# Kernel optimization log

Hardware: AMD Instinct MI355X
Metric: run time of the kernel (lower is better)

## Reference

```python
import jax, jax.numpy as jnp
import numpy as np

EMBED_DIM = 1024
NUM_HEADS = 16
HEAD_DIM = EMBED_DIM // NUM_HEADS


def setup_inputs() -> dict:
    key = jax.random.key(0)
    ks = jax.random.split(key, 11)
    B, S, E = 4, 2048, EMBED_DIM
    s = 1.0 / np.sqrt(E)
    return {
        "q": jax.random.normal(ks[0], (B, S, E), jnp.float32),
        "k": jax.random.normal(ks[1], (B, S, E), jnp.float32),
        "v": jax.random.normal(ks[2], (B, S, E), jnp.float32),
        "Wq": jax.random.uniform(ks[3], (E, E), jnp.float32, -s, s),
        "bq": jax.random.uniform(ks[4], (E,), jnp.float32, -s, s),
        "Wk": jax.random.uniform(ks[5], (E, E), jnp.float32, -s, s),
        "bk": jax.random.uniform(ks[6], (E,), jnp.float32, -s, s),
        "Wv": jax.random.uniform(ks[7], (E, E), jnp.float32, -s, s),
        "bv": jax.random.uniform(ks[8], (E,), jnp.float32, -s, s),
        "Wo": jax.random.uniform(ks[9], (E, E), jnp.float32, -s, s),
        "bo": jax.random.uniform(ks[10], (E,), jnp.float32, -s, s),
    }


def _split_heads(x):
    B, S, E = x.shape
    return x.reshape(B, S, NUM_HEADS, HEAD_DIM).transpose(0, 2, 1, 3)  # [B,H,S,D]


def reference(q, k, v, Wq, bq, Wk, bk, Wv, bv, Wo, bo):
    # torch Linear: x @ W.T + b
    Q = _split_heads(q @ Wq.T + bq)
    K = _split_heads(k @ Wk.T + bk)
    V = _split_heads(v @ Wv.T + bv)
    scale = 1.0 / jnp.sqrt(jnp.float32(HEAD_DIM))
    scores = jnp.einsum("bhqd,bhkd->bhqk", Q, K) * scale  # [B,H,S,S]
    weights = jax.nn.softmax(scores, axis=-1)
    ctx = jnp.einsum("bhqk,bhkd->bhqd", weights, V)
    B, H, S, D = ctx.shape
    merged = ctx.transpose(0, 2, 1, 3).reshape(B, S, H * D)
    out = merged @ Wo.T + bo
    return out, weights
```

## Files before the change

kernel.cpp:

```cpp
#include <hip/hip_runtime.h>
#include <hip/hip_bf16.h>

typedef __bf16 bf16x8 __attribute__((ext_vector_type(8)));
typedef float f32x4 __attribute__((ext_vector_type(4)));

constexpr size_t XQ_OFF = 0;
constexpr size_t XK_OFF = 8388608;
constexpr size_t XV_OFF = 16777216;
constexpr size_t WQ_OFF = 25165824;
constexpr size_t WK_OFF = 26214400;
constexpr size_t WV_OFF = 27262976;
constexpr size_t WO_OFF = 28311552;
constexpr size_t Q_OFF  = 29360128;
constexpr size_t KK_OFF = 37748736;
constexpr size_t VT_OFF = 46137344;
constexpr size_t CTX_OFF= 54525952;

__device__ __forceinline__ void gload16(const void* g, void* s) {
    __builtin_amdgcn_global_load_lds((__attribute__((address_space(1))) void*)g,
                                     (__attribute__((address_space(3))) void*)s, 16, 0, 0);
}

__global__ __launch_bounds__(256) void convert_k(
    const float* __restrict__ q, const float* __restrict__ k, const float* __restrict__ v,
    const float* __restrict__ Wq, const float* __restrict__ Wk, const float* __restrict__ Wv,
    const float* __restrict__ Wo, __bf16* __restrict__ ws) {
    int id = blockIdx.x * 256 + threadIdx.x;
    const int NX = 1048576;
    const int NW = 131072;
    const float* src; size_t dst; int local;
    if (id < 3 * NX) {
        int z = id / NX; local = id - z * NX;
        src = (z == 0) ? q : ((z == 1) ? k : v);
        dst = XQ_OFF + (size_t)z * 8388608;
    } else {
        int i2 = id - 3 * NX;
        int z = i2 / NW; local = i2 - z * NW;
        src = (z == 0) ? Wq : ((z == 1) ? Wk : ((z == 2) ? Wv : Wo));
        dst = WQ_OFF + (size_t)z * 1048576;
    }
    const float4* s4 = (const float4*)(src + (size_t)local * 8);
    float4 a = s4[0], b = s4[1];
    bf16x8 o;
    o[0]=(__bf16)a.x; o[1]=(__bf16)a.y; o[2]=(__bf16)a.z; o[3]=(__bf16)a.w;
    o[4]=(__bf16)b.x; o[5]=(__bf16)b.y; o[6]=(__bf16)b.z; o[7]=(__bf16)b.w;
    *(bf16x8*)(ws + dst + (size_t)local * 8) = o;
}

template<int MODE>
__global__ __launch_bounds__(256) void gemm_k(
    __bf16* __restrict__ ws,
    const float* __restrict__ bq, const float* __restrict__ bk,
    const float* __restrict__ bv, const float* __restrict__ bo,
    float* __restrict__ out) {
    const int K = 1024;
    int z = blockIdx.z;
    const __bf16* A; const __bf16* Bm; const float* bias;
    if (MODE == 0) {
        A    = ws + XQ_OFF + (size_t)z * 8388608;
        Bm   = ws + WQ_OFF + (size_t)z * 1048576;
        bias = (z == 0) ? bq : ((z == 1) ? bk : bv);
    } else {
        A    = ws + CTX_OFF;
        Bm   = ws + WO_OFF;
        bias = bo;
    }
    int row0 = blockIdx.x * 128, col0 = blockIdx.y * 128;
    __shared__ __align__(16) __bf16 As[128 * 32];
    __shared__ __align__(16) __bf16 Bs[128 * 32];
    int t = threadIdx.x, lane = t & 63, w = t >> 6;
    int wr = w >> 1, wc = w & 1;
    f32x4 acc[4][4];
#pragma unroll
    for (int i = 0; i < 4; ++i)
#pragma unroll
        for (int j = 0; j < 4; ++j) acc[i][j] = (f32x4){0.f, 0.f, 0.f, 0.f};

    for (int kt = 0; kt < K; kt += 32) {
#pragma unroll
        for (int i = 0; i < 2; ++i) {
            int e = ((i * 4 + w) * 64 + lane) * 8;
            int r = e >> 5, c = e & 31;
            gload16(A  + (size_t)(row0 + r) * K + kt + c, As + e);
            gload16(Bm + (size_t)(col0 + r) * K + kt + c, Bs + e);
        }
        __syncthreads();
        bf16x8 af[4], bfr[4];
#pragma unroll
        for (int f = 0; f < 4; ++f) {
            af[f]  = *(const bf16x8*)&As[(wr * 64 + f * 16 + (lane & 15)) * 32 + (lane >> 4) * 8];
            bfr[f] = *(const bf16x8*)&Bs[(wc * 64 + f * 16 + (lane & 15)) * 32 + (lane >> 4) * 8];
        }
#pragma unroll
        for (int fr = 0; fr < 4; ++fr)
#pragma unroll
            for (int fc = 0; fc < 4; ++fc)
                acc[fr][fc] = __builtin_amdgcn_mfma_f32_16x16x32_bf16(af[fr], bfr[fc], acc[fr][fc], 0, 0, 0);
        __syncthreads();
    }

    if (MODE == 0) {
        __bf16* dqk = ws + Q_OFF + (size_t)z * 8388608;
        __bf16* dvt = ws + VT_OFF;
#pragma unroll
        for (int fr = 0; fr < 4; ++fr)
#pragma unroll
            for (int fc = 0; fc < 4; ++fc)
#pragma unroll
                for (int r = 0; r < 4; ++r) {
                    int m = row0 + wr * 64 + fr * 16 + ((lane >> 4) << 2) + r;
                    int n = col0 + wc * 64 + fc * 16 + (lane & 15);
                    float val = acc[fr][fc][r] + bias[n];
                    int bb = m >> 11, s = m & 2047, h = n >> 6, d = n & 63;
                    size_t bh = (size_t)bb * 16 + h;
                    if (z < 2) dqk[bh * 131072 + (size_t)s * 64 + d] = (__bf16)val;
                    else       dvt[bh * 131072 + (size_t)d * 2048 + s] = (__bf16)val;
                }
    } else {
#pragma unroll
        for (int fr = 0; fr < 4; ++fr)
#pragma unroll
            for (int fc = 0; fc < 4; ++fc)
#pragma unroll
                for (int r = 0; r < 4; ++r) {
                    int m = row0 + wr * 64 + fr * 16 + ((lane >> 4) << 2) + r;
                    int n = col0 + wc * 64 + fc * 16 + (lane & 15);
                    out[(size_t)m * 1024 + n] = acc[fr][fc][r] + bias[n];
                }
    }
}

__global__ __launch_bounds__(256) void attn_k(const __bf16* __restrict__ ws,
                                              __bf16* __restrict__ wsw,
                                              float* __restrict__ wout) {
    const __bf16* Qp  = ws + Q_OFF;
    const __bf16* Kp  = ws + KK_OFF;
    const __bf16* Vtp = ws + VT_OFF;
    __bf16* ctx = wsw + CTX_OFF;

    int bh = blockIdx.y;
    int q0 = blockIdx.x * 64;
    int t = threadIdx.x, lane = t & 63, w = t >> 6;
    __shared__ __align__(16) __bf16 Qs[64 * 64];
    __shared__ __align__(16) __bf16 Ks[64 * 64];
    __shared__ __align__(16) __bf16 Vts[64 * 64];
    __shared__ __align__(16) __bf16 Ps[64 * 64];
    const float SCALE = 0.125f;

#pragma unroll
    for (int i = 0; i < 2; ++i) {
        int ch = t + 256 * i;
        int r = ch >> 3, c8 = ch & 7;
        bf16x8 val = *(const bf16x8*)&Qp[(size_t)bh * 131072 + (size_t)(q0 + r) * 64 + c8 * 8];
        *(bf16x8*)((char*)Qs + (r * 128 + ((c8 * 16) ^ ((r & 7) << 4)))) = val;
    }
    __syncthreads();
    int qrow = w * 16 + (lane & 15);
    bf16x8 aq0 = *(const bf16x8*)((char*)Qs + (qrow * 128 + (((lane >> 4) * 16)      ^ ((qrow & 7) << 4))));
    bf16x8 aq1 = *(const bf16x8*)((char*)Qs + (qrow * 128 + ((64 + (lane >> 4) * 16) ^ ((qrow & 7) << 4))));

    float rs[4] = {0.f, 0.f, 0.f, 0.f};
    for (int kt = 0; kt < 2048; kt += 64) {
        __syncthreads();
#pragma unroll
        for (int i = 0; i < 2; ++i) {
            int ch = t + 256 * i; int r = ch >> 3, c8 = ch & 7;
            bf16x8 val = *(const bf16x8*)&Kp[(size_t)bh * 131072 + (size_t)(kt + r) * 64 + c8 * 8];
            *(bf16x8*)((char*)Ks + (r * 128 + ((c8 * 16) ^ ((r & 7) << 4)))) = val;
        }
        __syncthreads();
#pragma unroll
        for (int kc = 0; kc < 4; ++kc) {
            int krow = kc * 16 + (lane & 15);
            bf16x8 b0 = *(const bf16x8*)((char*)Ks + (krow * 128 + (((lane >> 4) * 16)      ^ ((krow & 7) << 4))));
            bf16x8 b1 = *(const bf16x8*)((char*)Ks + (krow * 128 + ((64 + (lane >> 4) * 16) ^ ((krow & 7) << 4))));
            f32x4 s = (f32x4){0.f, 0.f, 0.f, 0.f};
            s = __builtin_amdgcn_mfma_f32_16x16x32_bf16(aq0, b0, s, 0, 0, 0);
            s = __builtin_amdgcn_mfma_f32_16x16x32_bf16(aq1, b1, s, 0, 0, 0);
#pragma unroll
            for (int r = 0; r < 4; ++r) rs[r] += __expf(s[r] * SCALE);
        }
    }
#pragma unroll
    for (int m = 1; m < 16; m <<= 1)
#pragma unroll
        for (int r = 0; r < 4; ++r) rs[r] += __shfl_xor(rs[r], m, 64);
    float rinv[4];
#pragma unroll
    for (int r = 0; r < 4; ++r) rinv[r] = 1.f / rs[r];

    f32x4 cacc[4];
#pragma unroll
    for (int i = 0; i < 4; ++i) cacc[i] = (f32x4){0.f, 0.f, 0.f, 0.f};

    for (int kt = 0; kt < 2048; kt += 64) {
        __syncthreads();
#pragma unroll
        for (int i = 0; i < 2; ++i) {
            int ch = t + 256 * i; int r = ch >> 3, c8 = ch & 7;
            bf16x8 kv = *(const bf16x8*)&Kp[(size_t)bh * 131072 + (size_t)(kt + r) * 64 + c8 * 8];
            *(bf16x8*)((char*)Ks + (r * 128 + ((c8 * 16) ^ ((r & 7) << 4)))) = kv;
            bf16x8 vv = *(const bf16x8*)&Vtp[(size_t)bh * 131072 + (size_t)r * 2048 + kt + c8 * 8];
            *(bf16x8*)((char*)Vts + (r * 128 + ((c8 * 16) ^ ((r & 7) << 4)))) = vv;
        }
        __syncthreads();
#pragma unroll
        for (int kc = 0; kc < 4; ++kc) {
            int krow = kc * 16 + (lane & 15);
            bf16x8 b0 = *(const bf16x8*)((char*)Ks + (krow * 128 + (((lane >> 4) * 16)      ^ ((krow & 7) << 4))));
            bf16x8 b1 = *(const bf16x8*)((char*)Ks + (krow * 128 + ((64 + (lane >> 4) * 16) ^ ((krow & 7) << 4))));
            f32x4 s = (f32x4){0.f, 0.f, 0.f, 0.f};
            s = __builtin_amdgcn_mfma_f32_16x16x32_bf16(aq0, b0, s, 0, 0, 0);
            s = __builtin_amdgcn_mfma_f32_16x16x32_bf16(aq1, b1, s, 0, 0, 0);
            float e[4];
#pragma unroll
            for (int r = 0; r < 4; ++r) e[r] = __expf(s[r] * SCALE) * rinv[r];
            size_t wbase = ((size_t)bh * 2048 + q0 + w * 16 + ((lane >> 4) << 2)) * 2048
                           + kt + kc * 16 + (lane & 15);
#pragma unroll
            for (int r = 0; r < 4; ++r) wout[wbase + (size_t)r * 2048] = e[r];
#pragma unroll
            for (int r = 0; r < 4; ++r) {
                int prow = w * 16 + ((lane >> 4) << 2) + r;
                int pcol = kc * 16 + (lane & 15);
                *(__bf16*)((char*)Ps + (prow * 128 + ((pcol * 2) ^ ((prow & 7) << 4)))) = (__bf16)e[r];
            }
        }
        __syncthreads();
#pragma unroll
        for (int ks = 0; ks < 2; ++ks) {
            int arow = w * 16 + (lane & 15);
            bf16x8 ap = *(const bf16x8*)((char*)Ps + (arow * 128 + ((ks * 64 + (lane >> 4) * 16) ^ ((arow & 7) << 4))));
#pragma unroll
            for (int dc = 0; dc < 4; ++dc) {
                int vrow = dc * 16 + (lane & 15);
                bf16x8 bv = *(const bf16x8*)((char*)Vts + (vrow * 128 + ((ks * 64 + (lane >> 4) * 16) ^ ((vrow & 7) << 4))));
                cacc[dc] = __builtin_amdgcn_mfma_f32_16x16x32_bf16(ap, bv, cacc[dc], 0, 0, 0);
            }
        }
    }

    int bb = bh >> 4, h = bh & 15;
#pragma unroll
    for (int dc = 0; dc < 4; ++dc)
#pragma unroll
        for (int r = 0; r < 4; ++r) {
            int qg = q0 + w * 16 + ((lane >> 4) << 2) + r;
            int d = dc * 16 + (lane & 15);
            ctx[((size_t)bb * 2048 + qg) * 1024 + h * 64 + d] = (__bf16)cacc[dc][r];
        }
}

extern "C" void kernel_launch(void* const* d_in, const int* in_sizes, int n_in,
                              void* d_out, int out_size, void* d_ws, size_t ws_size,
                              hipStream_t stream) {
    const float* q  = (const float*)d_in[0];
    const float* k  = (const float*)d_in[1];
    const float* v  = (const float*)d_in[2];
    const float* Wq = (const float*)d_in[3];
    const float* bq = (const float*)d_in[4];
    const float* Wk = (const float*)d_in[5];
    const float* bk = (const float*)d_in[6];
    const float* Wv = (const float*)d_in[7];
    const float* bv = (const float*)d_in[8];
    const float* Wo = (const float*)d_in[9];
    const float* bo = (const float*)d_in[10];
    __bf16* ws = (__bf16*)d_ws;
    float* out  = (float*)d_out;
    float* wout = out + 8388608;

    convert_k<<<dim3(14336), dim3(256), 0, stream>>>(q, k, v, Wq, Wk, Wv, Wo, ws);
    gemm_k<0><<<dim3(64, 8, 3), dim3(256), 0, stream>>>(ws, bq, bk, bv, bo, out);
    attn_k<<<dim3(32, 64), dim3(256), 0, stream>>>(ws, ws, wout);
    gemm_k<1><<<dim3(64, 8, 1), dim3(256), 0, stream>>>(ws, bq, bk, bv, bo, out);
}
```

Before: 558.0 us.

## Double-buffer GEMM and attention loads, remap blocks, widen attention tiles, coalesce weight writes

The GEMM now double-buffers its LDS tiles with async global-to-LDS loads and explicit waitcnt/barriers, and remaps block indices so neighbouring blocks share operands in cache. The attention kernel moves to 512 threads over 128 query rows and double-buffers K/V through direct-to-LDS loads. It also reuses the Q tile's LDS as the probability buffer and writes the fp32 weights as coalesced vector rows read back from LDS. These changes target load latency, synchronisation stalls and scattered weight stores. The cost is more LDS, fragile hand-written wait counts, and weights now rounded through bf16 before being stored.

New measurement: 580.0 us. +3.9%, slower.

```diff
diff --git a/kernel.cpp b/kernel.cpp
--- a/kernel.cpp
+++ b/kernel.cpp
@@ -5,12 +5,7 @@
 typedef float f32x4 __attribute__((ext_vector_type(4)));
 
 constexpr size_t XQ_OFF = 0;
-constexpr size_t XK_OFF = 8388608;
-constexpr size_t XV_OFF = 16777216;
 constexpr size_t WQ_OFF = 25165824;
-constexpr size_t WK_OFF = 26214400;
-constexpr size_t WV_OFF = 27262976;
-constexpr size_t WO_OFF = 28311552;
 constexpr size_t Q_OFF  = 29360128;
 constexpr size_t KK_OFF = 37748736;
 constexpr size_t VT_OFF = 46137344;
@@ -20,6 +15,10 @@
     __builtin_amdgcn_global_load_lds((__attribute__((address_space(1))) void*)g,
                                      (__attribute__((address_space(3))) void*)s, 16, 0, 0);
 }
+#define WAIT_VM0()   asm volatile("s_waitcnt vmcnt(0)" ::: "memory")
+#define WAIT_VM4()   asm volatile("s_waitcnt vmcnt(4)" ::: "memory")
+#define WAIT_LGKM0() asm volatile("s_waitcnt lgkmcnt(0)" ::: "memory")
+#define BAR()        __builtin_amdgcn_s_barrier()
 
 __global__ __launch_bounds__(256) void convert_k(
     const float* __restrict__ q, const float* __restrict__ k, const float* __restrict__ v,
@@ -54,7 +53,15 @@
     const float* __restrict__ bv, const float* __restrict__ bo,
     float* __restrict__ out) {
     const int K = 1024;
-    int z = blockIdx.z;
+    unsigned n = blockIdx.x + 64u * (blockIdx.y + 8u * blockIdx.z);
+    unsigned cpx = (MODE == 0) ? 192u : 64u;
+    unsigned m_ = (n & 7u) * cpx + (n >> 3);
+    unsigned bx = m_ & 63u;
+    unsigned rest = m_ >> 6;
+    unsigned by = rest & 7u;
+    unsigned bz = rest >> 3;
+
+    int z = (int)bz;
     const __bf16* A; const __bf16* Bm; const float* bias;
     if (MODE == 0) {
         A    = ws + XQ_OFF + (size_t)z * 8388608;
@@ -62,12 +69,12 @@
         bias = (z == 0) ? bq : ((z == 1) ? bk : bv);
     } else {
         A    = ws + CTX_OFF;
-        Bm   = ws + WO_OFF;
+        Bm   = ws + WQ_OFF + (size_t)3 * 1048576;
         bias = bo;
     }
-    int row0 = blockIdx.x * 128, col0 = blockIdx.y * 128;
-    __shared__ __align__(16) __bf16 As[128 * 32];
-    __shared__ __align__(16) __bf16 Bs[128 * 32];
+    int row0 = (int)bx * 128, col0 = (int)by * 128;
+    __shared__ __align__(16) __bf16 As[2][128 * 32];
+    __shared__ __align__(16) __bf16 Bs[2][128 * 32];
     int t = threadIdx.x, lane = t & 63, w = t >> 6;
     int wr = w >> 1, wc = w & 1;
     f32x4 acc[4][4];
@@ -76,27 +83,39 @@
 #pragma unroll
         for (int j = 0; j < 4; ++j) acc[i][j] = (f32x4){0.f, 0.f, 0.f, 0.f};
 
-    for (int kt = 0; kt < K; kt += 32) {
+    auto stage = [&](int buf, int kt) {
 #pragma unroll
         for (int i = 0; i < 2; ++i) {
             int e = ((i * 4 + w) * 64 + lane) * 8;
             int r = e >> 5, c = e & 31;
-            gload16(A  + (size_t)(row0 + r) * K + kt + c, As + e);
-            gload16(Bm + (size_t)(col0 + r) * K + kt + c, Bs + e);
-        }
-        __syncthreads();
+            gload16(A  + (size_t)(row0 + r) * K + kt + c, &As[buf][e]);
+            gload16(Bm + (size_t)(col0 + r) * K + kt + c, &Bs[buf][e]);
+        }
+    };
+
+    stage(0, 0);
+    int cur = 0;
+    for (int kt = 0; kt < K; kt += 32) {
+        bool nx = kt + 32 < K;
+        if (nx) { stage(cur ^ 1, kt + 32); WAIT_VM4(); }
+        else    { WAIT_VM0(); }
+        BAR();
+        const __bf16* Ac = As[cur];
+        const __bf16* Bc = Bs[cur];
         bf16x8 af[4], bfr[4];
 #pragma unroll
         for (int f = 0; f < 4; ++f) {
-            af[f]  = *(const bf16x8*)&As[(wr * 64 + f * 16 + (lane & 15)) * 32 + (lane >> 4) * 8];
-            bfr[f] = *(const bf16x8*)&Bs[(wc * 64 + f * 16 + (lane & 15)) * 32 + (lane >> 4) * 8];
+            af[f]  = *(const bf16x8*)&Ac[(wr * 64 + f * 16 + (lane & 15)) * 32 + (lane >> 4) * 8];
+            bfr[f] = *(const bf16x8*)&Bc[(wc * 64 + f * 16 + (lane & 15)) * 32 + (lane >> 4) * 8];
         }
 #pragma unroll
         for (int fr = 0; fr < 4; ++fr)
 #pragma unroll
             for (int fc = 0; fc < 4; ++fc)
                 acc[fr][fc] = __builtin_amdgcn_mfma_f32_16x16x32_bf16(af[fr], bfr[fc], acc[fr][fc], 0, 0, 0);
-        __syncthreads();
+        WAIT_LGKM0();
+        BAR();
+        cur ^= 1;
     }
 
     if (MODE == 0) {
@@ -109,9 +128,9 @@
 #pragma unroll
                 for (int r = 0; r < 4; ++r) {
                     int m = row0 + wr * 64 + fr * 16 + ((lane >> 4) << 2) + r;
-                    int n = col0 + wc * 64 + fc * 16 + (lane & 15);
-                    float val = acc[fr][fc][r] + bias[n];
-                    int bb = m >> 11, s = m & 2047, h = n >> 6, d = n & 63;
+                    int nn = col0 + wc * 64 + fc * 16 + (lane & 15);
+                    float val = acc[fr][fc][r] + bias[nn];
+                    int bb = m >> 11, s = m & 2047, h = nn >> 6, d = nn & 63;
                     size_t bh = (size_t)bb * 16 + h;
                     if (z < 2) dqk[bh * 131072 + (size_t)s * 64 + d] = (__bf16)val;
                     else       dvt[bh * 131072 + (size_t)d * 2048 + s] = (__bf16)val;
@@ -124,13 +143,13 @@
 #pragma unroll
                 for (int r = 0; r < 4; ++r) {
                     int m = row0 + wr * 64 + fr * 16 + ((lane >> 4) << 2) + r;
-                    int n = col0 + wc * 64 + fc * 16 + (lane & 15);
-                    out[(size_t)m * 1024 + n] = acc[fr][fc][r] + bias[n];
+                    int nn = col0 + wc * 64 + fc * 16 + (lane & 15);
+                    out[(size_t)m * 1024 + nn] = acc[fr][fc][r] + bias[nn];
                 }
     }
 }
 
-__global__ __launch_bounds__(256) void attn_k(const __bf16* __restrict__ ws,
+__global__ __launch_bounds__(512) void attn_k(const __bf16* __restrict__ ws,
                                               __bf16* __restrict__ wsw,
                                               float* __restrict__ wout) {
     const __bf16* Qp  = ws + Q_OFF;
@@ -138,116 +157,141 @@
     const __bf16* Vtp = ws + VT_OFF;
     __bf16* ctx = wsw + CTX_OFF;
 
-    int bh = blockIdx.y;
-    int q0 = blockIdx.x * 64;
-    int t = threadIdx.x, lane = t & 63, w = t >> 6;
-    __shared__ __align__(16) __bf16 Qs[64 * 64];
-    __shared__ __align__(16) __bf16 Ks[64 * 64];
-    __shared__ __align__(16) __bf16 Vts[64 * 64];
-    __shared__ __align__(16) __bf16 Ps[64 * 64];
+    unsigned n = blockIdx.x + 16u * blockIdx.y;
+    int bh = (int)((n & 7u) * 8u + ((n >> 3) >> 4));
+    int q0 = (int)((n >> 3) & 15u) * 128;
+
+    int t = threadIdx.x, lane = t & 63, w = t >> 6, g = lane >> 4;
+    __shared__ __align__(16) __bf16 QP[128 * 64];
+    __shared__ __align__(16) __bf16 Ks[2][64 * 64];
+    __shared__ __align__(16) __bf16 Vts[2][64 * 64];
+    const __bf16* Qb = Qp  + (size_t)bh * 131072;
+    const __bf16* Kb = Kp  + (size_t)bh * 131072;
+    const __bf16* Vb = Vtp + (size_t)bh * 131072;
     const float SCALE = 0.125f;
 
 #pragma unroll
     for (int i = 0; i < 2; ++i) {
-        int ch = t + 256 * i;
-        int r = ch >> 3, c8 = ch & 7;
-        bf16x8 val = *(const bf16x8*)&Qp[(size_t)bh * 131072 + (size_t)(q0 + r) * 64 + c8 * 8];
-        *(bf16x8*)((char*)Qs + (r * 128 + ((c8 * 16) ^ ((r & 7) << 4)))) = val;
-    }
-    __syncthreads();
+        int ch = t + 512 * i, r = ch >> 3, c8 = ch & 7;
+        gload16(Qb + (size_t)(q0 + r) * 64 + ((c8 ^ (r & 7)) << 3), &QP[ch * 8]);
+    }
+    WAIT_VM0(); BAR();
     int qrow = w * 16 + (lane & 15);
-    bf16x8 aq0 = *(const bf16x8*)((char*)Qs + (qrow * 128 + (((lane >> 4) * 16)      ^ ((qrow & 7) << 4))));
-    bf16x8 aq1 = *(const bf16x8*)((char*)Qs + (qrow * 128 + ((64 + (lane >> 4) * 16) ^ ((qrow & 7) << 4))));
-
+    bf16x8 aq0 = *(const bf16x8*)((const char*)QP + qrow * 128 + ((g * 16) ^ ((qrow & 7) << 4)));
+    bf16x8 aq1 = *(const bf16x8*)((const char*)QP + qrow * 128 + (((4 + g) * 16) ^ ((qrow & 7) << 4)));
+
+    {
+        int r = t >> 3, c8 = t & 7;
+        gload16(Kb + (size_t)r * 64 + ((c8 ^ (r & 7)) << 3), &Ks[0][t * 8]);
+    }
+    WAIT_VM0(); BAR();
     float rs[4] = {0.f, 0.f, 0.f, 0.f};
+    int cur = 0;
     for (int kt = 0; kt < 2048; kt += 64) {
-        __syncthreads();
-#pragma unroll
-        for (int i = 0; i < 2; ++i) {
-            int ch = t + 256 * i; int r = ch >> 3, c8 = ch & 7;
-            bf16x8 val = *(const bf16x8*)&Kp[(size_t)bh * 131072 + (size_t)(kt + r) * 64 + c8 * 8];
-            *(bf16x8*)((char*)Ks + (r * 128 + ((c8 * 16) ^ ((r & 7) << 4)))) = val;
-        }
-        __syncthreads();
+        bool nx = kt < 1984;
+        if (nx) {
+            int r = t >> 3, c8 = t & 7;
+            gload16(Kb + (size_t)(kt + 64 + r) * 64 + ((c8 ^ (r & 7)) << 3), &Ks[cur ^ 1][t * 8]);
+        }
+        const __bf16* Kc = Ks[cur];
 #pragma unroll
         for (int kc = 0; kc < 4; ++kc) {
             int krow = kc * 16 + (lane & 15);
-            bf16x8 b0 = *(const bf16x8*)((char*)Ks + (krow * 128 + (((lane >> 4) * 16)      ^ ((krow & 7) << 4))));
-            bf16x8 b1 = *(const bf16x8*)((char*)Ks + (krow * 128 + ((64 + (lane >> 4) * 16) ^ ((krow & 7) << 4))));
+            bf16x8 b0 = *(const bf16x8*)((const char*)Kc + krow * 128 + ((g * 16) ^ ((krow & 7) << 4)));
+            bf16x8 b1 = *(const bf16x8*)((const char*)Kc + krow * 128 + (((4 + g) * 16) ^ ((krow & 7) << 4)));
             f32x4 s = (f32x4){0.f, 0.f, 0.f, 0.f};
             s = __builtin_amdgcn_mfma_f32_16x16x32_bf16(aq0, b0, s, 0, 0, 0);
             s = __builtin_amdgcn_mfma_f32_16x16x32_bf16(aq1, b1, s, 0, 0, 0);
 #pragma unroll
-            for (int r = 0; r < 4; ++r) rs[r] += __expf(s[r] * SCALE);
-        }
+            for (int r4 = 0; r4 < 4; ++r4) rs[r4] += __expf(s[r4] * SCALE);
+        }
+        WAIT_LGKM0();
+        if (nx) WAIT_VM0();
+        BAR();
+        cur ^= 1;
     }
 #pragma unroll
     for (int m = 1; m < 16; m <<= 1)
 #pragma unroll
-        for (int r = 0; r < 4; ++r) rs[r] += __shfl_xor(rs[r], m, 64);
+        for (int r4 = 0; r4 < 4; ++r4) rs[r4] += __shfl_xor(rs[r4], m);
     float rinv[4];
 #pragma unroll
-    for (int r = 0; r < 4; ++r) rinv[r] = 1.f / rs[r];
-
+    for (int r4 = 0; r4 < 4; ++r4) rinv[r4] = 1.f / rs[r4];
+
+    {
+        int r = t >> 3, c8 = t & 7;
+        gload16(Kb + (size_t)r * 64   + ((c8 ^ (r & 7)) << 3), &Ks[0][t * 8]);
+        gload16(Vb + (size_t)r * 2048 + ((c8 ^ (r & 7)) << 3), &Vts[0][t * 8]);
+    }
+    WAIT_VM0(); BAR();
+    cur = 0;
     f32x4 cacc[4];
 #pragma unroll
     for (int i = 0; i < 4; ++i) cacc[i] = (f32x4){0.f, 0.f, 0.f, 0.f};
 
     for (int kt = 0; kt < 2048; kt += 64) {
-        __syncthreads();
-#pragma unroll
-        for (int i = 0; i < 2; ++i) {
-            int ch = t + 256 * i; int r = ch >> 3, c8 = ch & 7;
-            bf16x8 kv = *(const bf16x8*)&Kp[(size_t)bh * 131072 + (size_t)(kt + r) * 64 + c8 * 8];
-            *(bf16x8*)((char*)Ks + (r * 128 + ((c8 * 16) ^ ((r & 7) << 4)))) = kv;
-            bf16x8 vv = *(const bf16x8*)&Vtp[(size_t)bh * 131072 + (size_t)r * 2048 + kt + c8 * 8];
-            *(bf16x8*)((char*)Vts + (r * 128 + ((c8 * 16) ^ ((r & 7) << 4)))) = vv;
-        }
-        __syncthreads();
+        bool nx = kt < 1984;
+        if (nx) {
+            int r = t >> 3, c8 = t & 7;
+            gload16(Kb + (size_t)(kt + 64 + r) * 64 + ((c8 ^ (r & 7)) << 3), &Ks[cur ^ 1][t * 8]);
+            gload16(Vb + (size_t)r * 2048 + (kt + 64) + ((c8 ^ (r & 7)) << 3), &Vts[cur ^ 1][t * 8]);
+        }
+        const __bf16* Kc = Ks[cur];
+        const __bf16* Vc = Vts[cur];
 #pragma unroll
         for (int kc = 0; kc < 4; ++kc) {
             int krow = kc * 16 + (lane & 15);
-            bf16x8 b0 = *(const bf16x8*)((char*)Ks + (krow * 128 + (((lane >> 4) * 16)      ^ ((krow & 7) << 4))));
-            bf16x8 b1 = *(const bf16x8*)((char*)Ks + (krow * 128 + ((64 + (lane >> 4) * 16) ^ ((krow & 7) << 4))));
+            bf16x8 b0 = *(const bf16x8*)((const char*)Kc + krow * 128 + ((g * 16) ^ ((krow & 7) << 4)));
+            bf16x8 b1 = *(const bf16x8*)((const char*)Kc + krow * 128 + (((4 + g) * 16) ^ ((krow & 7) << 4)));
             f32x4 s = (f32x4){0.f, 0.f, 0.f, 0.f};
             s = __builtin_amdgcn_mfma_f32_16x16x32_bf16(aq0, b0, s, 0, 0, 0);
             s = __builtin_amdgcn_mfma_f32_16x16x32_bf16(aq1, b1, s, 0, 0, 0);
-            float e[4];
-#pragma unroll
-            for (int r = 0; r < 4; ++r) e[r] = __expf(s[r] * SCALE) * rinv[r];
-            size_t wbase = ((size_t)bh * 2048 + q0 + w * 16 + ((lane >> 4) << 2)) * 2048
-                           + kt + kc * 16 + (lane & 15);
-#pragma unroll
-            for (int r = 0; r < 4; ++r) wout[wbase + (size_t)r * 2048] = e[r];
-#pragma unroll
-            for (int r = 0; r < 4; ++r) {
-                int prow = w * 16 + ((lane >> 4) << 2) + r;
+#pragma unroll
+            for (int r4 = 0; r4 < 4; ++r4) {
+                float e = __expf(s[r4] * SCALE) * rinv[r4];
+                int prow = w * 16 + (g << 2) + r4;
                 int pcol = kc * 16 + (lane & 15);
-                *(__bf16*)((char*)Ps + (prow * 128 + ((pcol * 2) ^ ((prow & 7) << 4)))) = (__bf16)e[r];
+                *(__bf16*)((char*)QP + prow * 128 + ((pcol * 2) ^ ((prow & 7) << 4))) = (__bf16)e;
             }
         }
-        __syncthreads();
+        WAIT_LGKM0();
+        __builtin_amdgcn_sched_barrier(0);
+        BAR();
+#pragma unroll
+        for (int i = 0; i < 2; ++i) {
+            int ch = t + 512 * i, row = ch >> 3, c8 = ch & 7;
+            bf16x8 p = *(const bf16x8*)((const char*)QP + row * 128 + ((c8 * 16) ^ ((row & 7) << 4)));
+            f32x4 lo = (f32x4){(float)p[0], (float)p[1], (float)p[2], (float)p[3]};
+            f32x4 hi = (f32x4){(float)p[4], (float)p[5], (float)p[6], (float)p[7]};
+            float* dst = wout + ((size_t)bh * 2048 + q0 + row) * 2048 + kt + c8 * 8;
+            *(f32x4*)dst = lo;
+            *(f32x4*)(dst + 4) = hi;
+        }
+        int arow = w * 16 + (lane & 15);
 #pragma unroll
         for (int ks = 0; ks < 2; ++ks) {
-            int arow = w * 16 + (lane & 15);
-            bf16x8 ap = *(const bf16x8*)((char*)Ps + (arow * 128 + ((ks * 64 + (lane >> 4) * 16) ^ ((arow & 7) << 4))));
+            bf16x8 ap = *(const bf16x8*)((const char*)QP + arow * 128 + ((ks * 64 + g * 16) ^ ((arow & 7) << 4)));
 #pragma unroll
             for (int dc = 0; dc < 4; ++dc) {
                 int vrow = dc * 16 + (lane & 15);
-                bf16x8 bv = *(const bf16x8*)((char*)Vts + (vrow * 128 + ((ks * 64 + (lane >> 4) * 16) ^ ((vrow & 7) << 4))));
+                bf16x8 bv = *(const bf16x8*)((const char*)Vc + vrow * 128 + ((ks * 64 + g * 16) ^ ((vrow & 7) << 4)));
                 cacc[dc] = __builtin_amdgcn_mfma_f32_16x16x32_bf16(ap, bv, cacc[dc], 0, 0, 0);
             }
         }
+        WAIT_LGKM0();
+        if (nx) WAIT_VM0();
+        BAR();
+        cur ^= 1;
     }
 
     int bb = bh >> 4, h = bh & 15;
 #pragma unroll
     for (int dc = 0; dc < 4; ++dc)
 #pragma unroll
-        for (int r = 0; r < 4; ++r) {
-            int qg = q0 + w * 16 + ((lane >> 4) << 2) + r;
+        for (int r4 = 0; r4 < 4; ++r4) {
+            int qg = q0 + w * 16 + (g << 2) + r4;
             int d = dc * 16 + (lane & 15);
-            ctx[((size_t)bb * 2048 + qg) * 1024 + h * 64 + d] = (__bf16)cacc[dc][r];
+            ctx[((size_t)bb * 2048 + qg) * 1024 + h * 64 + d] = (__bf16)cacc[dc][r4];
         }
 }
 
@@ -271,6 +315,6 @@
 
     convert_k<<<dim3(14336), dim3(256), 0, stream>>>(q, k, v, Wq, Wk, Wv, Wo, ws);
     gemm_k<0><<<dim3(64, 8, 3), dim3(256), 0, stream>>>(ws, bq, bk, bv, bo, out);
-    attn_k<<<dim3(32, 64), dim3(256), 0, stream>>>(ws, ws, wout);
+    attn_k<<<dim3(16, 64), dim3(512), 0, stream>>>(ws, ws, wout);
     gemm_k<1><<<dim3(64, 8, 1), dim3(256), 0, stream>>>(ws, bq, bk, bv, bo, out);
 }
```
